# Kernel optimization log

Hardware: AMD Instinct MI355X
Metric: run time of the kernel (lower is better)

Reference implementation:

```python
import jax, jax.numpy as jnp
import numpy as np


def setup_inputs() -> dict:
    key = jax.random.key(0)
    k1, k2, k3 = jax.random.split(key, 3)
    C, H, W = 64, 512, 512
    D, K = 128, 3
    input = jax.random.normal(k1, (C, H, W), dtype=jnp.float32)
    # He-style init as in the module
    kernels = jax.random.normal(k2, (D, C, K, K), dtype=jnp.float32) * jnp.sqrt(2.0 / (C * K * K))
    biases = jax.random.normal(k3, (D, H - K + 1, W - K + 1), dtype=jnp.float32)
    return {"input": input, "kernels": kernels, "biases": biases}


def reference(input, kernels, biases):
    # valid 2D cross-correlation summed over input channels, plus per-pixel bias
    # input: [C,H,W], kernels: [D,C,k,k], biases: [D,H-k+1,W-k+1]
    x = input[None]  # [1,C,H,W]
    out = jax.lax.conv_general_dilated(
        x, kernels,
        window_strides=(1, 1),
        padding="VALID",
        dimension_numbers=("NCHW", "OIHW", "NCHW"),
    )[0]  # [D,H-k+1,W-k+1]; lax conv is cross-correlation, matching correlate2d
    return out + biases
```

## Files before the change

### kernel.cpp

```cpp
#include <hip/hip_runtime.h>
#include <hip/hip_bf16.h>

#define C_IN 64
#define H_IN 512
#define W_IN 512
#define D_OUT 128
#define OH 510
#define OW 510

typedef __bf16 bf16x8 __attribute__((ext_vector_type(8)));
typedef float  f32x4  __attribute__((ext_vector_type(4)));
typedef float  f32x2  __attribute__((ext_vector_type(2)));

#define TIN_ELEMS (H_IN * W_IN * C_IN)
#define TIN_BYTES ((size_t)TIN_ELEMS * 2)
#define WT_BYTES  (9 * D_OUT * C_IN * 2)
#define WS_NEEDED (TIN_BYTES + WT_BYTES)

__global__ void prep_weights(const float* __restrict__ w, __bf16* __restrict__ wt) {
    int i = blockIdx.x * blockDim.x + threadIdx.x;
    if (i >= 9 * D_OUT * C_IN) return;
    int c    = i & 63;
    int d    = (i >> 6) & 127;
    int kpos = i >> 13;
    wt[i] = (__bf16)w[((d * C_IN) + c) * 9 + kpos];
}

__global__ __launch_bounds__(256, 4)
void transpose_in(const float* __restrict__ in, __bf16* __restrict__ tin) {
    __shared__ float ls[32 * 257];
    const int b    = blockIdx.x;
    const int y    = b >> 2;
    const int px0  = ((b >> 1) & 1) << 8;
    const int cc   = b & 1;
    const int t    = threadIdx.x;
    const int wave = t >> 6;
    const int lane = t & 63;

#pragma unroll
    for (int j = 0; j < 8; j++) {
        const int cl = wave * 8 + j;
        f32x4 v = *(const f32x4*)&in[(cc * 32 + cl) * (H_IN * W_IN) + y * W_IN + px0 + lane * 4];
        *(f32x4*)&ls[cl * 257 + lane * 4] = v;
    }
    __syncthreads();
    const int oct = t & 3;
    const int pxw = t >> 2;
#pragma unroll
    for (int pass = 0; pass < 4; pass++) {
        const int pxl = pass * 64 + pxw;
        bf16x8 v;
#pragma unroll
        for (int j = 0; j < 8; j++)
            v[j] = (__bf16)ls[(oct * 8 + j) * 257 + pxl];
        *(bf16x8*)&tin[((size_t)(y * W_IN) + px0 + pxl) * C_IN + cc * 32 + oct * 8] = v;
    }
}

#define BPX 256
#define LO_STRIDE 260

__global__ __launch_bounds__(512, 6)
void conv_main(const __bf16* __restrict__ tin, const __bf16* __restrict__ wt,
               const float* __restrict__ bias, float* __restrict__ out) {
    __shared__ __align__(16) char smem[9 * 32 * 64 * 2];
    __bf16* lw = (__bf16*)smem;
    float*  lo = (float*)smem;

    const int bid = blockIdx.x;
    const int swz = (bid & 7) * 255 + (bid >> 3);
    const int dt  = swz & 3;
    const int xt  = (swz >> 2) & 1;
    const int y   = (swz >> 3) << 1;
    const int d0  = dt << 5;
    const int x0  = xt ? (OW - BPX) : 0;

    const int t    = threadIdx.x;
    const int wave = t >> 6;
    const int lane = t & 63;
    const int l15  = lane & 15;
    const int quad = lane >> 4;
    const int wr   = wave >> 2;
    const int wp   = wave & 3;

    for (int u = t; u < 9 * 32 * 8; u += 512) {
        const int kpos = u >> 8;
        const int r    = u & 255;
        const int dl   = r >> 3;
        const int oc   = r & 7;
        const int ocs  = (oc ^ (dl & 7)) * 8;
        bf16x8 v = *(const bf16x8*)(wt + kpos * (D_OUT * C_IN) + (d0 + dl) * C_IN + oc * 8);
        *(bf16x8*)&lw[(kpos * 32 + dl) * 64 + ocs] = v;
    }
    __syncthreads();

    f32x4 acc[4][2];
#pragma unroll
    for (int pxg = 0; pxg < 4; pxg++)
#pragma unroll
        for (int dg = 0; dg < 2; dg++)
            acc[pxg][dg] = (f32x4){0.f, 0.f, 0.f, 0.f};

    const __bf16* tb = tin + ((size_t)(y + wr) * W_IN + x0 + wp * 64) * C_IN + quad * 8;
#pragma unroll
    for (int kpos = 0; kpos < 9; kpos++) {
        const int ky = kpos / 3, kx = kpos % 3;
#pragma unroll
        for (int ch = 0; ch < 2; ch++) {
            const int us = (((ch * 4 + quad) ^ (l15 & 7)) * 8);
            bf16x8 w0 = *(const bf16x8*)&lw[(kpos * 32 + l15) * 64 + us];
            bf16x8 w1 = *(const bf16x8*)&lw[(kpos * 32 + 16 + l15) * 64 + us];
            const __bf16* base = tb + ((size_t)ky * W_IN + kx) * C_IN + ch * 32;
#pragma unroll
            for (int pxg = 0; pxg < 4; pxg++) {
                bf16x8 pf = *(const bf16x8*)(base + (pxg * 16 + l15) * C_IN);
                acc[pxg][0] = __builtin_amdgcn_mfma_f32_16x16x32_bf16(pf, w0, acc[pxg][0], 0, 0, 0);
                acc[pxg][1] = __builtin_amdgcn_mfma_f32_16x16x32_bf16(pf, w1, acc[pxg][1], 0, 0, 0);
            }
        }
    }

    const size_t OHW = (size_t)OH * OW;
    const size_t obase = (size_t)(d0 + wave * 4) * OHW + (size_t)y * OW + x0 + lane * 4;
    f32x2 bp[4][2];
#pragma unroll
    for (int i = 0; i < 4; i++) {
        bp[i][0] = *(const f32x2*)&bias[obase + (size_t)i * OHW];
        bp[i][1] = *(const f32x2*)&bias[obase + (size_t)i * OHW + 2];
    }
#pragma unroll
    for (int i = 0; i < 4; i++) asm volatile("" : "+v"(bp[i][0]), "+v"(bp[i][1]));

    __syncthreads();

    if (wr == 0) {
#pragma unroll
        for (int pxg = 0; pxg < 4; pxg++)
#pragma unroll
            for (int dg = 0; dg < 2; dg++)
                *(f32x4*)&lo[(dg * 16 + l15) * LO_STRIDE + wp * 64 + pxg * 16 + quad * 4] = acc[pxg][dg];
    }
    __syncthreads();

    f32x2 bn[4][2];
#pragma unroll
    for (int i = 0; i < 4; i++) {
        bn[i][0] = *(const f32x2*)&bias[obase + (size_t)i * OHW + OW];
        bn[i][1] = *(const f32x2*)&bias[obase + (size_t)i * OHW + OW + 2];
    }

#pragma unroll
    for (int i = 0; i < 4; i++) {
        f32x4 v = *(const f32x4*)&lo[(wave * 4 + i) * LO_STRIDE + lane * 4];
        const size_t o = obase + (size_t)i * OHW;
        f32x2 r0 = { v[0] + bp[i][0][0], v[1] + bp[i][0][1] };
        f32x2 r1 = { v[2] + bp[i][1][0], v[3] + bp[i][1][1] };
        *(f32x2*)&out[o]     = r0;
        *(f32x2*)&out[o + 2] = r1;
    }
    __syncthreads();

    if (wr == 1) {
#pragma unroll
        for (int pxg = 0; pxg < 4; pxg++)
#pragma unroll
            for (int dg = 0; dg < 2; dg++)
                *(f32x4*)&lo[(dg * 16 + l15) * LO_STRIDE + wp * 64 + pxg * 16 + quad * 4] = acc[pxg][dg];
    }
    __syncthreads();

#pragma unroll
    for (int i = 0; i < 4; i++) {
        f32x4 v = *(const f32x4*)&lo[(wave * 4 + i) * LO_STRIDE + lane * 4];
        const size_t o = obase + (size_t)i * OHW + OW;
        f32x2 r0 = { v[0] + bn[i][0][0], v[1] + bn[i][0][1] };
        f32x2 r1 = { v[2] + bn[i][1][0], v[3] + bn[i][1][1] };
        *(f32x2*)&out[o]     = r0;
        *(f32x2*)&out[o + 2] = r1;
    }
}

#define PXT 64
#define TCOL 66
#define TCPAD 72

__global__ __launch_bounds__(256, 4)
void conv_bias_fallback(const float* __restrict__ in, const __bf16* __restrict__ wt,
                        const float* __restrict__ bias, float* __restrict__ out) {
    __shared__ __bf16 tile[3 * TCOL * TCPAD];
    const int b  = blockIdx.x;
    const int y  = b >> 3;
    const int x0 = (b & 7) * PXT;
    const int tid = threadIdx.x;
    for (int idx = tid; idx < 3 * TCOL * C_IN; idx += 256) {
        int col = idx % TCOL;
        int t   = idx / TCOL;
        int r   = t % 3;
        int c   = t / 3;
        int gx  = x0 + col;
        if (gx > W_IN - 1) gx = W_IN - 1;
        tile[(r * TCOL + col) * TCPAD + c] = (__bf16)in[(c * H_IN + (y + r)) * W_IN + gx];
    }
    __syncthreads();
    const int wave = tid >> 6, lane = tid & 63;
    const int l15 = lane & 15, quad = lane >> 4;
    const int px_base = wave * 16;
    f32x4 acc[8];
#pragma unroll
    for (int i = 0; i < 8; i++) acc[i] = (f32x4){0.f, 0.f, 0.f, 0.f};
#pragma unroll
    for (int kpos = 0; kpos < 9; kpos++) {
        const int ky = kpos / 3, kx = kpos % 3;
#pragma unroll
        for (int ch = 0; ch < 2; ch++) {
            const int c0 = ch * 32;
            bf16x8 bfrag = *(const bf16x8*)&tile[(ky * TCOL + px_base + l15 + kx) * TCPAD + c0 + quad * 8];
            const __bf16* aptr = wt + (size_t)kpos * D_OUT * C_IN + l15 * C_IN + c0 + quad * 8;
#pragma unroll
            for (int ds = 0; ds < 8; ds++) {
                bf16x8 afrag = *(const bf16x8*)(aptr + ds * 16 * C_IN);
                acc[ds] = __builtin_amdgcn_mfma_f32_16x16x32_bf16(afrag, bfrag, acc[ds], 0, 0, 0);
            }
        }
    }
    const int gx = x0 + px_base + l15;
    if (gx < OW) {
#pragma unroll
        for (int ds = 0; ds < 8; ds++) {
            const int dbase = ds * 16 + quad * 4;
#pragma unroll
            for (int r = 0; r < 4; r++) {
                const size_t o = ((size_t)(dbase + r) * OH + y) * OW + gx;
                out[o] = acc[ds][r] + bias[o];
            }
        }
    }
}

extern "C" void kernel_launch(void* const* d_in, const int* in_sizes, int n_in,
                              void* d_out, int out_size, void* d_ws, size_t ws_size,
                              hipStream_t stream) {
    const float* in   = (const float*)d_in[0];
    const float* w    = (const float*)d_in[1];
    const float* bias = (const float*)d_in[2];
    float* out = (float*)d_out;

    if (ws_size >= WS_NEEDED) {
        __bf16* tin = (__bf16*)d_ws;
        __bf16* wt  = (__bf16*)((char*)d_ws + TIN_BYTES);
        prep_weights<<<(9 * D_OUT * C_IN + 255) / 256, 256, 0, stream>>>(w, wt);
        transpose_in<<<H_IN * 4, 256, 0, stream>>>(in, tin);
        conv_main<<<(OH / 2) * 8, 512, 0, stream>>>(tin, wt, bias, out);
    } else {
        __bf16* wt = (__bf16*)d_ws;
        prep_weights<<<(9 * D_OUT * C_IN + 255) / 256, 256, 0, stream>>>(w, wt);
        conv_bias_fallback<<<OH * 8, 256, 0, stream>>>(in, wt, bias, out);
    }
}
```

Before: 418.9 us.

## Prefetch conv input fragments with triple buffering and simplify input transpose

The conv main loop is rewritten as 18 (kpos, channel-half) steps. Global loads for step b+2 are issued before the MFMAs of step b, using a rotating three-slot register buffer so load latency is hidden behind matrix math. The occupancy hint for conv_main drops from 6 to 4 to leave room for the extra registers. The input transpose kernel no longer stages through shared memory: each thread reads 16 channels for one pixel directly, converts them, and writes two 16-byte vectors. Reads stay coalesced across pixels, but the kernel now launches many more small blocks.

Measured after the change: 411.0 us. About the same (-1.9%).

```diff
diff --git a/kernel.cpp b/kernel.cpp
--- a/kernel.cpp
+++ b/kernel.cpp
@@ -26,41 +26,49 @@
     wt[i] = (__bf16)w[((d * C_IN) + c) * 9 + kpos];
 }
 
-__global__ __launch_bounds__(256, 4)
+__global__ __launch_bounds__(256, 8)
 void transpose_in(const float* __restrict__ in, __bf16* __restrict__ tin) {
-    __shared__ float ls[32 * 257];
-    const int b    = blockIdx.x;
-    const int y    = b >> 2;
-    const int px0  = ((b >> 1) & 1) << 8;
-    const int cc   = b & 1;
-    const int t    = threadIdx.x;
-    const int wave = t >> 6;
-    const int lane = t & 63;
-
-#pragma unroll
-    for (int j = 0; j < 8; j++) {
-        const int cl = wave * 8 + j;
-        f32x4 v = *(const f32x4*)&in[(cc * 32 + cl) * (H_IN * W_IN) + y * W_IN + px0 + lane * 4];
-        *(f32x4*)&ls[cl * 257 + lane * 4] = v;
-    }
-    __syncthreads();
-    const int oct = t & 3;
-    const int pxw = t >> 2;
-#pragma unroll
-    for (int pass = 0; pass < 4; pass++) {
-        const int pxl = pass * 64 + pxw;
-        bf16x8 v;
-#pragma unroll
-        for (int j = 0; j < 8; j++)
-            v[j] = (__bf16)ls[(oct * 8 + j) * 257 + pxl];
-        *(bf16x8*)&tin[((size_t)(y * W_IN) + px0 + pxl) * C_IN + cc * 32 + oct * 8] = v;
-    }
+    const int t  = threadIdx.x;
+    const int w  = t >> 6;
+    const int l  = t & 63;
+    const int px = blockIdx.x * 64 + l;
+    const float* src = in + (size_t)(w * 16) * (H_IN * W_IN) + px;
+    float f[16];
+#pragma unroll
+    for (int j = 0; j < 16; j++) f[j] = src[(size_t)j * (H_IN * W_IN)];
+    bf16x8 v0, v1;
+#pragma unroll
+    for (int j = 0; j < 8; j++) { v0[j] = (__bf16)f[j]; v1[j] = (__bf16)f[8 + j]; }
+    __bf16* dst = tin + (size_t)px * C_IN + w * 16;
+    *(bf16x8*)dst       = v0;
+    *(bf16x8*)(dst + 8) = v1;
 }
 
 #define BPX 256
 #define LO_STRIDE 260
 
-__global__ __launch_bounds__(512, 6)
+#define LOADB(buf, kpos_, ch_)                                                    \
+  { const int ky_ = (kpos_) / 3, kx_ = (kpos_) % 3;                               \
+    const __bf16* base_ = tb + ((size_t)ky_ * W_IN + kx_) * C_IN + (ch_) * 32;    \
+    buf[0] = *(const bf16x8*)(base_ + ( 0 + l15) * C_IN);                         \
+    buf[1] = *(const bf16x8*)(base_ + (16 + l15) * C_IN);                         \
+    buf[2] = *(const bf16x8*)(base_ + (32 + l15) * C_IN);                         \
+    buf[3] = *(const bf16x8*)(base_ + (48 + l15) * C_IN); }
+
+#define MFMAB(buf, kpos_, ch_)                                                    \
+  { const int us_ = (((ch_) * 4 + quad) ^ (l15 & 7)) * 8;                         \
+    bf16x8 w0_ = *(const bf16x8*)&lw[((kpos_) * 32      + l15) * 64 + us_];       \
+    bf16x8 w1_ = *(const bf16x8*)&lw[((kpos_) * 32 + 16 + l15) * 64 + us_];       \
+    acc[0][0] = __builtin_amdgcn_mfma_f32_16x16x32_bf16(buf[0], w0_, acc[0][0], 0, 0, 0); \
+    acc[0][1] = __builtin_amdgcn_mfma_f32_16x16x32_bf16(buf[0], w1_, acc[0][1], 0, 0, 0); \
+    acc[1][0] = __builtin_amdgcn_mfma_f32_16x16x32_bf16(buf[1], w0_, acc[1][0], 0, 0, 0); \
+    acc[1][1] = __builtin_amdgcn_mfma_f32_16x16x32_bf16(buf[1], w1_, acc[1][1], 0, 0, 0); \
+    acc[2][0] = __builtin_amdgcn_mfma_f32_16x16x32_bf16(buf[2], w0_, acc[2][0], 0, 0, 0); \
+    acc[2][1] = __builtin_amdgcn_mfma_f32_16x16x32_bf16(buf[2], w1_, acc[2][1], 0, 0, 0); \
+    acc[3][0] = __builtin_amdgcn_mfma_f32_16x16x32_bf16(buf[3], w0_, acc[3][0], 0, 0, 0); \
+    acc[3][1] = __builtin_amdgcn_mfma_f32_16x16x32_bf16(buf[3], w1_, acc[3][1], 0, 0, 0); }
+
+__global__ __launch_bounds__(512, 4)
 void conv_main(const __bf16* __restrict__ tin, const __bf16* __restrict__ wt,
                const float* __restrict__ bias, float* __restrict__ out) {
     __shared__ __align__(16) char smem[9 * 32 * 64 * 2];
@@ -102,22 +110,14 @@
             acc[pxg][dg] = (f32x4){0.f, 0.f, 0.f, 0.f};
 
     const __bf16* tb = tin + ((size_t)(y + wr) * W_IN + x0 + wp * 64) * C_IN + quad * 8;
-#pragma unroll
-    for (int kpos = 0; kpos < 9; kpos++) {
-        const int ky = kpos / 3, kx = kpos % 3;
-#pragma unroll
-        for (int ch = 0; ch < 2; ch++) {
-            const int us = (((ch * 4 + quad) ^ (l15 & 7)) * 8);
-            bf16x8 w0 = *(const bf16x8*)&lw[(kpos * 32 + l15) * 64 + us];
-            bf16x8 w1 = *(const bf16x8*)&lw[(kpos * 32 + 16 + l15) * 64 + us];
-            const __bf16* base = tb + ((size_t)ky * W_IN + kx) * C_IN + ch * 32;
-#pragma unroll
-            for (int pxg = 0; pxg < 4; pxg++) {
-                bf16x8 pf = *(const bf16x8*)(base + (pxg * 16 + l15) * C_IN);
-                acc[pxg][0] = __builtin_amdgcn_mfma_f32_16x16x32_bf16(pf, w0, acc[pxg][0], 0, 0, 0);
-                acc[pxg][1] = __builtin_amdgcn_mfma_f32_16x16x32_bf16(pf, w1, acc[pxg][1], 0, 0, 0);
-            }
-        }
+
+    bf16x8 pbuf[3][4];
+    LOADB(pbuf[0], 0, 0);
+    LOADB(pbuf[1], 0, 1);
+#pragma unroll
+    for (int b2 = 0; b2 < 18; ++b2) {
+        if (b2 < 16) LOADB(pbuf[(b2 + 2) % 3], (b2 + 2) >> 1, (b2 + 2) & 1);
+        MFMAB(pbuf[b2 % 3], b2 >> 1, b2 & 1);
     }
 
     const size_t OHW = (size_t)OH * OW;
@@ -249,7 +249,7 @@
         __bf16* tin = (__bf16*)d_ws;
         __bf16* wt  = (__bf16*)((char*)d_ws + TIN_BYTES);
         prep_weights<<<(9 * D_OUT * C_IN + 255) / 256, 256, 0, stream>>>(w, wt);
-        transpose_in<<<H_IN * 4, 256, 0, stream>>>(in, tin);
+        transpose_in<<<(H_IN * W_IN) / 64, 256, 0, stream>>>(in, tin);
         conv_main<<<(OH / 2) * 8, 512, 0, stream>>>(tin, wt, bias, out);
     } else {
         __bf16* wt = (__bf16*)d_ws;
```
